# Optimization experiments

Measured on AMD Instinct MI355X. Metric: run time of the kernel, lower is better.

## Reference

```python
import jax, jax.numpy as jnp
import numpy as np

UNITS = 1024
IN_DIM = 1024
BATCH = 64
SEQ = 512


def setup_inputs() -> dict:
    key = jax.random.key(0)
    k_x, k_wf, k_wb = jax.random.split(key, 3)
    x = jax.random.normal(k_x, (BATCH, SEQ, IN_DIM), dtype=jnp.float32)
    # keras 'random_normal' initializer -> stddev 0.05
    W_fwd = jax.random.normal(k_wf, (IN_DIM + UNITS, 4 * UNITS), dtype=jnp.float32) * 0.05
    b_fwd = jnp.zeros((4 * UNITS,), dtype=jnp.float32)
    W_bwd = jax.random.normal(k_wb, (IN_DIM + UNITS, 4 * UNITS), dtype=jnp.float32) * 0.05
    b_bwd = jnp.zeros((4 * UNITS,), dtype=jnp.float32)
    return {"x": x, "W_fwd": W_fwd, "b_fwd": b_fwd, "W_bwd": W_bwd, "b_bwd": b_bwd}


def _lstm_scan(x_tbd, W, b, units, reverse):
    # x_tbd: [T, B, D] time-major
    B = x_tbd.shape[1]
    h0 = jnp.zeros((B, units), dtype=x_tbd.dtype)
    c0 = jnp.zeros((B, units), dtype=x_tbd.dtype)

    def step(carry, x_t):
        h, c = carry
        z = jnp.concatenate([x_t, h], axis=-1) @ W + b  # [B, 4U]
        zi, zf, zo, zg = jnp.split(z, 4, axis=-1)
        c_new = jax.nn.sigmoid(zf) * c + jax.nn.sigmoid(zi) * jnp.tanh(zg)
        h_new = jax.nn.sigmoid(zo) * jnp.tanh(c_new)
        return (h_new, c_new), h_new

    _, hs = jax.lax.scan(step, (h0, c0), x_tbd, reverse=reverse)
    return hs  # [T, B, U], aligned with input time order


def reference(x, W_fwd, b_fwd, W_bwd, b_bwd):
    x_tbd = jnp.transpose(x, (1, 0, 2))  # [T, B, D]
    h_fwd = _lstm_scan(x_tbd, W_fwd, b_fwd, UNITS, reverse=False)
    h_bwd = _lstm_scan(x_tbd, W_bwd, b_bwd, UNITS, reverse=True)
    h = jnp.concatenate([h_fwd, h_bwd], axis=-1)  # [T, B, 2U]
    return jnp.transpose(h, (1, 0, 2))  # [B, T, 2U]
```

## Files before the change

kernel.cpp:

```cpp
#include <hip/hip_runtime.h>
#include <stdint.h>

#define B_ 64
#define T_ 512
#define D_ 1024
#define U_ 1024
#define G4_ 4096
#define M_ (B_ * T_)

typedef unsigned short u16;
typedef float f32x4 __attribute__((ext_vector_type(4)));
typedef _Float16 f16x8 __attribute__((ext_vector_type(8)));
typedef unsigned short u16x4 __attribute__((ext_vector_type(4)));

__device__ __forceinline__ u16 f2h(float f) {
  union { _Float16 h; u16 u; } v; v.h = (_Float16)f; return v.u;
}
__device__ __forceinline__ float h2f(u16 u) {
  union { _Float16 h; u16 u; } v; v.u = u; return (float)v.h;
}
__device__ __forceinline__ float sigm(float x) { return 1.f / (1.f + __expf(-x)); }
__device__ __forceinline__ float tanhf_(float x) {
  x = fminf(12.f, fmaxf(-12.f, x));
  float e = __expf(2.f * x);
  return (e - 1.f) / (e + 1.f);
}

__device__ __forceinline__ void glds16(const void* g, void* l) {
  __builtin_amdgcn_global_load_lds(
      (const __attribute__((address_space(1))) uint32_t*)g,
      (__attribute__((address_space(3))) uint32_t*)l, 16, 0, 0);
}

template <int R>
__device__ __forceinline__ void stage_tile(const char* gbase, long gs, char* lds, int tid) {
  const int lane = tid & 63, wid = tid >> 6;
#pragma unroll
  for (int j = wid; j < R / 8; j += 4) {
    const int row = j * 8 + (lane >> 3);
    const int lg = ((lane & 7) * 16) ^ ((row & 7) << 4);
    glds16(gbase + (long)row * gs + lg, lds + j * 1024);
  }
}

__device__ __forceinline__ f16x8 read_frag(const char* lds, int row, int kbyte) {
  const int ph = row * 128 + (kbyte ^ ((row & 7) << 4));
  return *(const f16x8*)(lds + ph);
}

#define MFMA_(a, b, c) __builtin_amdgcn_mfma_f32_16x16x32_f16(a, b, c, 0, 0, 0)

#define BAR_LGKM() asm volatile("s_waitcnt lgkmcnt(0)\n\ts_barrier" ::: "memory")


__global__ __launch_bounds__(256) void cast_x_kernel(const float* __restrict__ x,
                                                     u16* __restrict__ xb) {
  const long n = (long)M_ * D_ / 4;
  for (long i = (long)blockIdx.x * blockDim.x + threadIdx.x; i < n;
       i += (long)gridDim.x * blockDim.x) {
    f32x4 v = ((const f32x4*)x)[i];
    u16x4 r;
#pragma unroll
    for (int j = 0; j < 4; ++j) r[j] = f2h(v[j]);
    ((u16x4*)xb)[i] = r;
  }
}

__global__ __launch_bounds__(256) void pack_w_kernel(const float* __restrict__ Wf,
                                                     const float* __restrict__ Wb,
                                                     u16* __restrict__ wxT,
                                                     u16* __restrict__ whT) {
  const int idx = blockIdx.x * 256 + threadIdx.x;
  const int p = idx & 4095;
  const int kc = (idx >> 12) & 63;
  const int part = (idx >> 18) & 1;
  const int d = (idx >> 19) & 1;
  const float* W = d ? Wb : Wf;
  const int orig = ((p >> 4) & 3) * 1024 + ((p >> 6) << 4) + (p & 15);
  u16* dst = (part ? whT : wxT) + ((long)d * G4_ + p) * 1024 + kc * 16;
  const float* src = W + ((long)(part * 1024 + kc * 16)) * G4_ + orig;
#pragma unroll
  for (int j = 0; j < 16; ++j) dst[j] = f2h(src[(long)j * G4_]);
}

__global__ __launch_bounds__(256) void gemm_xproj2(const u16* __restrict__ xbf,
                                                   const u16* __restrict__ wT,
                                                   const float* __restrict__ bF,
                                                   const float* __restrict__ bB,
                                                   u16* __restrict__ xp2) {
  __shared__ __align__(16) char smem[64 * 1024];
  const int tid = threadIdx.x, lane = tid & 63, wid = tid >> 6;
  const int wr = wid >> 1, wc = wid & 1;
  const int tm = blockIdx.x * 128, tn = blockIdx.y * 128, d = blockIdx.z;
  const char* Ag = (const char*)xbf + (long)tm * 2048;
  const char* Bg = (const char*)wT + ((long)d * G4_ + tn) * 2048;

  f32x4 acc[4][4];
#pragma unroll
  for (int mi = 0; mi < 4; ++mi)
#pragma unroll
    for (int ni = 0; ni < 4; ++ni)
#pragma unroll
      for (int v = 0; v < 4; ++v) acc[mi][ni][v] = 0.f;

  stage_tile<128>(Ag, 2048, smem, tid);
  stage_tile<128>(Bg, 2048, smem + 32768, tid);
  __syncthreads();
  const int rA = lane & 15, kb = (lane >> 4) * 16;

  for (int cc = 0; cc < 16; ++cc) {
    const int cur = cc & 1;
    char* Ac = smem + cur * 16384;
    char* Bc = smem + 32768 + cur * 16384;
    if (cc + 1 < 16) {
      stage_tile<128>(Ag + (cc + 1) * 128, 2048, smem + (cur ^ 1) * 16384, tid);
      stage_tile<128>(Bg + (cc + 1) * 128, 2048, smem + 32768 + (cur ^ 1) * 16384, tid);
    }
    f16x8 aF[4][2], bFr[4][2];
#pragma unroll
    for (int mi = 0; mi < 4; ++mi)
#pragma unroll
      for (int ks = 0; ks < 2; ++ks)
        aF[mi][ks] = read_frag(Ac, wr * 64 + mi * 16 + rA, kb + ks * 64);
#pragma unroll
    for (int ni = 0; ni < 4; ++ni)
#pragma unroll
      for (int ks = 0; ks < 2; ++ks)
        bFr[ni][ks] = read_frag(Bc, wc * 64 + ni * 16 + rA, kb + ks * 64);
#pragma unroll
    for (int mi = 0; mi < 4; ++mi)
#pragma unroll
      for (int ni = 0; ni < 4; ++ni)
#pragma unroll
        for (int ks = 0; ks < 2; ++ks)
          acc[mi][ni] = MFMA_(aF[mi][ks], bFr[ni][ks], acc[mi][ni]);
    __syncthreads();
  }

  const float* bias = d ? bB : bF;
#pragma unroll
  for (int ni = 0; ni < 4; ++ni) {
    const int p = tn + wc * 64 + ni * 16 + rA;
    const int orig = ((p >> 4) & 3) * 1024 + ((p >> 6) << 4) + (p & 15);
    const float bv = bias[orig];
    const int ub2 = p >> 6, pl = p & 63;
#pragma unroll
    for (int mi = 0; mi < 4; ++mi) {
      const int m0 = tm + wr * 64 + mi * 16 + (lane >> 4) * 4;
#pragma unroll
      for (int v = 0; v < 4; ++v) {
        const int m = m0 + v, b = m >> 9, t = m & 511;
        xp2[((((long)d * T_ + t) * 64 + ub2) * 64 + b) * 64 + pl] =
            f2h(acc[mi][ni][v] + bv);
      }
    }
  }
}

__global__ __launch_bounds__(512) void lstm_persist(
    const u16* __restrict__ whT, const u16* __restrict__ xp2,
    u16* __restrict__ hst, float* __restrict__ out, uint32_t* flags) {
  __shared__ __align__(16) char smem[147456];
  float* zbuf = (float*)(smem + 131072);
  const int tid = threadIdx.x, lane = tid & 63, wid = tid >> 6;
  const int bx = blockIdx.x, d = bx & 1, ub = bx >> 1;
  const int wm = wid & 3, kh = wid >> 2, rA = lane & 15, kq = lane >> 4;

  {
    const char* wbase = (const char*)(whT + ((long)d * G4_ + ub * 64) * 1024);
#pragma unroll
    for (int q = 0; q < 16; ++q) {
      const int idx = wid * 16 + q;
      const int row = idx >> 1;
      const int jl = (idx & 1) * 1024 + lane * 16;
      glds16(wbase + (long)row * 2048 + (jl ^ ((row & 7) << 4)), smem + idx * 1024);
    }
  }
  asm volatile("s_waitcnt vmcnt(0)" ::: "memory");
  __syncthreads();

  const int b_g = tid >> 3, up_g = tid & 7;
  const int u_g = ub * 16 + up_g * 2;
  float creg0 = 0.f, creg1 = 0.f;
  uint32_t* fl = flags + (long)d * 64 * 4;

  for (int s = 0; s < T_; ++s) {
    const int t = d ? (T_ - 1 - s) : s;

    if (wid == 0) {
      const uint32_t* fp = fl + lane * 4;
      int it = 0;
      while (true) {
        uint32_t v;
        asm volatile("global_load_dword %0, %1, off sc0 sc1\n\ts_waitcnt vmcnt(0)"
                     : "=v"(v) : "v"(fp) : "memory");
        if (__all(v >= (uint32_t)s)) break;
        __builtin_amdgcn_s_sleep(1);
        if (++it > (1 << 17)) break;
      }
    }
    BAR_LGKM();

    const u16* hr = hst + (long)(s & 1) * 131072 + d * 65536;
    const char* abase =
        (const char*)(hr + ((long)(wm * 16 + rA)) * 1024) + kh * 1024 + kq * 16;
    f16x8 areg[16];
#define ALOAD(i)                                                        \
  asm volatile("global_load_dwordx4 %0, %1, off offset:%2 sc0 sc1"     \
               : "=v"(areg[i]) : "v"(abase), "n"(i * 64) : "memory")
    ALOAD(0); ALOAD(1); ALOAD(2); ALOAD(3);
    ALOAD(4); ALOAD(5); ALOAD(6); ALOAD(7);
    ALOAD(8); ALOAD(9); ALOAD(10); ALOAD(11);
    ALOAD(12); ALOAD(13); ALOAD(14); ALOAD(15);
#undef ALOAD
    const u16* xb0 = xp2 + ((((long)d * T_ + t) * 64 + ub) * 64 + b_g) * 64 + up_g * 2;
    uint32_t xr[4];
#define XLOAD(g)                                                        \
  asm volatile("global_load_dword %0, %1, off offset:%2"               \
               : "=v"(xr[g]) : "v"(xb0), "n"(g * 32) : "memory")
    XLOAD(0); XLOAD(1); XLOAD(2); XLOAD(3);
#undef XLOAD
    asm volatile("s_waitcnt vmcnt(4)" ::: "memory");
    __builtin_amdgcn_sched_barrier(0);

    f32x4 acc[4];
#pragma unroll
    for (int ni = 0; ni < 4; ++ni)
#pragma unroll
      for (int v = 0; v < 4; ++v) acc[ni][v] = 0.f;
#pragma unroll
    for (int kk = 0; kk < 16; ++kk) {
      const int kbyte = kh * 1024 + kk * 64 + kq * 16;
#pragma unroll
      for (int ni = 0; ni < 4; ++ni) {
        const int pi = ni * 16 + rA;
        const f16x8 bF =
            *(const f16x8*)(smem + pi * 2048 + (kbyte ^ ((pi & 7) << 4)));
        acc[ni] = MFMA_(areg[kk], bF, acc[ni]);
      }
    }

    if (kh == 1) {
#pragma unroll
      for (int ni = 0; ni < 4; ++ni)
#pragma unroll
        for (int v = 0; v < 4; ++v)
          zbuf[(wm * 16 + kq * 4 + v) * 64 + ni * 16 + rA] = acc[ni][v];
    }
    BAR_LGKM();
    if (kh == 0) {
#pragma unroll
      for (int ni = 0; ni < 4; ++ni)
#pragma unroll
        for (int v = 0; v < 4; ++v) {
          const int ix = (wm * 16 + kq * 4 + v) * 64 + ni * 16 + rA;
          zbuf[ix] += acc[ni][v];
        }
    }
    BAR_LGKM();

    asm volatile("s_waitcnt vmcnt(0)" ::: "memory");
    __builtin_amdgcn_sched_barrier(0);

    const float* zb = zbuf + b_g * 64 + up_g * 2;
    const float zi0 = zb[0]  + h2f((u16)(xr[0] & 0xffff));
    const float zi1 = zb[1]  + h2f((u16)(xr[0] >> 16));
    const float zf0 = zb[16] + h2f((u16)(xr[1] & 0xffff));
    const float zf1 = zb[17] + h2f((u16)(xr[1] >> 16));
    const float zo0 = zb[32] + h2f((u16)(xr[2] & 0xffff));
    const float zo1 = zb[33] + h2f((u16)(xr[2] >> 16));
    const float zg0 = zb[48] + h2f((u16)(xr[3] & 0xffff));
    const float zg1 = zb[49] + h2f((u16)(xr[3] >> 16));
    const float cn0 = sigm(zf0) * creg0 + sigm(zi0) * tanhf_(zg0);
    const float cn1 = sigm(zf1) * creg1 + sigm(zi1) * tanhf_(zg1);
    const float hn0 = sigm(zo0) * tanhf_(cn0);
    const float hn1 = sigm(zo1) * tanhf_(cn1);
    creg0 = cn0; creg1 = cn1;

    u16* hw = hst + (long)((s + 1) & 1) * 131072 + d * 65536;
    const uint32_t hv = (uint32_t)f2h(hn0) | ((uint32_t)f2h(hn1) << 16);
    u16* hptr = hw + (long)b_g * 1024 + u_g;
    asm volatile("global_store_dword %0, %1, off sc0 sc1"
                 :: "v"(hptr), "v"(hv) : "memory");
    asm volatile("s_waitcnt vmcnt(0)" ::: "memory");
    BAR_LGKM();
    if (tid == 0) {
      const uint32_t fv = (uint32_t)(s + 1);
      uint32_t* fp2 = fl + ub * 4;
      asm volatile("global_store_dword %0, %1, off sc0 sc1"
                   :: "v"(fp2), "v"(fv) : "memory");
    }

    float2 o2; o2.x = hn0; o2.y = hn1;
    *(float2*)(out + ((long)b_g * T_ + t) * 2048 + d * 1024 + u_g) = o2;
  }
}

__global__ __launch_bounds__(256) void lstm_step_fused(
    const u16* __restrict__ whT, const u16* __restrict__ wxT,
    const u16* __restrict__ xbf,
    const float* __restrict__ bF, const float* __restrict__ bB,
    const u16* __restrict__ h_read, u16* __restrict__ h_write,
    float* __restrict__ c_state, float* __restrict__ out, int s) {
  __shared__ __align__(16) char smem[32 * 1024];
  float* zbuf = (float*)smem;
  const int tid = threadIdx.x, lane = tid & 63, wid = tid >> 6;
  const int wr = wid >> 1, wc = wid & 1;
  const int ub = blockIdx.x, d = blockIdx.y;
  const int t = d ? (T_ - 1 - s) : s;
  const char* hA = (const char*)(h_read + (long)d * B_ * U_);
  const char* Bh = (const char*)(whT + ((long)d * G4_ + ub * 64) * 1024);
  const char* xA = (const char*)xbf + (long)t * (D_ * 2);
  const char* Bx = (const char*)(wxT + ((long)d * G4_ + ub * 64) * 1024);

  auto stage = [&](int cc, int buf) {
    char* Ad = smem + buf * 8192;
    char* Bd = smem + 16384 + buf * 8192;
    if (cc < 16) {
      stage_tile<64>(hA + cc * 128, U_ * 2, Ad, tid);
      stage_tile<64>(Bh + cc * 128, 1024 * 2, Bd, tid);
    } else {
      const int cx = cc - 16;
      stage_tile<64>(xA + cx * 128, (long)T_ * D_ * 2, Ad, tid);
      stage_tile<64>(Bx + cx * 128, 1024 * 2, Bd, tid);
    }
  };

  f32x4 acc[2][2];
#pragma unroll
  for (int mi = 0; mi < 2; ++mi)
#pragma unroll
    for (int ni = 0; ni < 2; ++ni)
#pragma unroll
      for (int v = 0; v < 4; ++v) acc[mi][ni][v] = 0.f;

  stage(0, 0);
  __syncthreads();
  const int rA = lane & 15, kb = (lane >> 4) * 16;

  for (int cc = 0; cc < 32; ++cc) {
    const int cur = cc & 1;
    char* Ac = smem + cur * 8192;
    char* Bc = smem + 16384 + cur * 8192;
    if (cc + 1 < 32) stage(cc + 1, cur ^ 1);
    f16x8 aF[2][2], bFr[2][2];
#pragma unroll
    for (int mi = 0; mi < 2; ++mi)
#pragma unroll
      for (int ks = 0; ks < 2; ++ks)
        aF[mi][ks] = read_frag(Ac, wr * 32 + mi * 16 + rA, kb + ks * 64);
#pragma unroll
    for (int ni = 0; ni < 2; ++ni)
#pragma unroll
      for (int ks = 0; ks < 2; ++ks)
        bFr[ni][ks] = read_frag(Bc, wc * 32 + ni * 16 + rA, kb + ks * 64);
#pragma unroll
    for (int mi = 0; mi < 2; ++mi)
#pragma unroll
      for (int ni = 0; ni < 2; ++ni)
#pragma unroll
        for (int ks = 0; ks < 2; ++ks)
          acc[mi][ni] = MFMA_(aF[mi][ks], bFr[ni][ks], acc[mi][ni]);
    __syncthreads();
  }

#pragma unroll
  for (int mi = 0; mi < 2; ++mi)
#pragma unroll
    for (int ni = 0; ni < 2; ++ni)
#pragma unroll
      for (int v = 0; v < 4; ++v) {
        const int row = wr * 32 + mi * 16 + (lane >> 4) * 4 + v;
        const int col = wc * 32 + ni * 16 + rA;
        zbuf[row * 64 + col] = acc[mi][ni][v];
      }
  __syncthreads();

  const int b = tid >> 2, u0 = (tid & 3) * 4;
  const float* bias = d ? bB : bF;
#pragma unroll
  for (int j = 0; j < 4; ++j) {
    const int ui = u0 + j, u = ub * 16 + ui;
    float zi = zbuf[b * 64 + ui] + bias[u];
    float zf = zbuf[b * 64 + 16 + ui] + bias[1024 + u];
    float zo = zbuf[b * 64 + 32 + ui] + bias[2048 + u];
    float zg = zbuf[b * 64 + 48 + ui] + bias[3072 + u];
    const long ci = (((long)d * B_ + b) << 10) + u;
    const float c = c_state[ci];
    const float i_ = sigm(zi), ff = sigm(zf), o_ = sigm(zo), g_ = tanhf_(zg);
    const float cn = ff * c + i_ * g_;
    const float hn = o_ * tanhf_(cn);
    c_state[ci] = cn;
    h_write[ci] = f2h(hn);
    out[(((long)b * T_ + t) << 11) + ((long)d << 10) + u] = hn;
  }
}


extern "C" void kernel_launch(void* const* d_in, const int* in_sizes, int n_in,
                              void* d_out, int out_size, void* d_ws, size_t ws_size,
                              hipStream_t stream) {
  const float* x = (const float*)d_in[0];
  const float* Wf = (const float*)d_in[1];
  const float* bfp = (const float*)d_in[2];
  const float* Wb = (const float*)d_in[3];
  const float* bbp = (const float*)d_in[4];
  float* out = (float*)d_out;
  char* ws = (char*)d_ws;

  size_t off = 0;
  auto alloc = [&](size_t bytes) {
    char* p = ws + off;
    off = (off + bytes + 255) & ~(size_t)255;
    return p;
  };
  u16* xbf = (u16*)alloc((size_t)M_ * D_ * 2);
  u16* wxT = (u16*)alloc((size_t)2 * G4_ * 1024 * 2);
  u16* whT = (u16*)alloc((size_t)2 * G4_ * 1024 * 2);
  u16* hst = (u16*)alloc((size_t)2 * 2 * B_ * U_ * 2);
  float* cst = (float*)alloc((size_t)2 * B_ * U_ * 4);
  uint32_t* flags = (uint32_t*)alloc((size_t)2 * 64 * 16 * 4);
  const size_t base_need = off;
  const size_t xproj_bytes = (size_t)2 * B_ * T_ * G4_ * 2;
  const bool fused = (ws_size < base_need + xproj_bytes + 256);
  u16* xproj = fused ? nullptr : (u16*)alloc(xproj_bytes);

  hipMemsetAsync(hst, 0, (size_t)2 * 2 * B_ * U_ * 2, stream);
  hipMemsetAsync(flags, 0, (size_t)2 * 64 * 16 * 4, stream);

  cast_x_kernel<<<2048, 256, 0, stream>>>(x, xbf);
  pack_w_kernel<<<4096, 256, 0, stream>>>(Wf, Wb, wxT, whT);

  if (!fused) {
    dim3 gg(M_ / 128, G4_ / 128, 2);
    gemm_xproj2<<<gg, 256, 0, stream>>>(xbf, wxT, bfp, bbp, xproj);
    lstm_persist<<<128, 512, 0, stream>>>(whT, xproj, hst, out, flags);
  } else {
    hipMemsetAsync(cst, 0, (size_t)2 * B_ * U_ * 4, stream);
    for (int s = 0; s < T_; ++s) {
      const u16* hr = hst + (size_t)(s & 1) * 2 * B_ * U_;
      u16* hw = hst + (size_t)((s + 1) & 1) * 2 * B_ * U_;
      lstm_step_fused<<<dim3(64, 2), 256, 0, stream>>>(whT, wxT, xbf, bfp, bbp,
                                                       hr, hw, cst, out, s);
    }
  }
}
```

Baseline: 4.451 ms.

## Version hidden-state buffers per step and relayout recurrent weights in LDS

```diff
diff --git a/kernel.cpp b/kernel.cpp
--- a/kernel.cpp
+++ b/kernel.cpp
@@ -157,10 +157,12 @@
   }
 }
 
+#define ZLD 65
+template <int VER>
 __global__ __launch_bounds__(512) void lstm_persist(
     const u16* __restrict__ whT, const u16* __restrict__ xp2,
     u16* __restrict__ hst, float* __restrict__ out, uint32_t* flags) {
-  __shared__ __align__(16) char smem[147456];
+  __shared__ __align__(16) char smem[131072 + ZLD * 64 * 4];
   float* zbuf = (float*)(smem + 131072);
   const int tid = threadIdx.x, lane = tid & 63, wid = tid >> 6;
   const int bx = blockIdx.x, d = bx & 1, ub = bx >> 1;
@@ -170,10 +172,11 @@
     const char* wbase = (const char*)(whT + ((long)d * G4_ + ub * 64) * 1024);
 #pragma unroll
     for (int q = 0; q < 16; ++q) {
-      const int idx = wid * 16 + q;
-      const int row = idx >> 1;
-      const int jl = (idx & 1) * 1024 + lane * 16;
-      glds16(wbase + (long)row * 2048 + (jl ^ ((row & 7) << 4)), smem + idx * 1024);
+      const int f = wid * 16 + q;
+      const int ni = f >> 5, kkg = f & 31;
+      const int row = ni * 16 + (lane & 15);
+      glds16(wbase + (long)row * 2048 + kkg * 64 + (lane >> 4) * 16,
+             smem + f * 1024);
     }
   }
   asm volatile("s_waitcnt vmcnt(0)" ::: "memory");
@@ -186,6 +189,14 @@
 
   for (int s = 0; s < T_; ++s) {
     const int t = d ? (T_ - 1 - s) : s;
+
+    const u16* xb0 = xp2 + ((((long)d * T_ + t) * 64 + ub) * 64 + b_g) * 64 + up_g * 2;
+    uint32_t xr[4];
+#define XLOAD(g)                                                        \
+  asm volatile("global_load_dword %0, %1, off offset:%2"               \
+               : "=v"(xr[g]) : "v"(xb0), "n"(g * 32) : "memory")
+    XLOAD(0); XLOAD(1); XLOAD(2); XLOAD(3);
+#undef XLOAD
 
     if (wid == 0) {
       const uint32_t* fp = fl + lane * 4;
@@ -201,26 +212,31 @@
     }
     BAR_LGKM();
 
-    const u16* hr = hst + (long)(s & 1) * 131072 + d * 65536;
+    const u16* hr = hst + (VER ? (long)s * 131072 : (long)(s & 1) * 131072)
+                    + (long)d * 65536;
     const char* abase =
         (const char*)(hr + ((long)(wm * 16 + rA)) * 1024) + kh * 1024 + kq * 16;
     f16x8 areg[16];
-#define ALOAD(i)                                                        \
+#define ALOADC(i)                                                       \
+  asm volatile("global_load_dwordx4 %0, %1, off offset:%2"             \
+               : "=v"(areg[i]) : "v"(abase), "n"(i * 64) : "memory")
+#define ALOADU(i)                                                       \
   asm volatile("global_load_dwordx4 %0, %1, off offset:%2 sc0 sc1"     \
                : "=v"(areg[i]) : "v"(abase), "n"(i * 64) : "memory")
-    ALOAD(0); ALOAD(1); ALOAD(2); ALOAD(3);
-    ALOAD(4); ALOAD(5); ALOAD(6); ALOAD(7);
-    ALOAD(8); ALOAD(9); ALOAD(10); ALOAD(11);
-    ALOAD(12); ALOAD(13); ALOAD(14); ALOAD(15);
-#undef ALOAD
-    const u16* xb0 = xp2 + ((((long)d * T_ + t) * 64 + ub) * 64 + b_g) * 64 + up_g * 2;
-    uint32_t xr[4];
-#define XLOAD(g)                                                        \
-  asm volatile("global_load_dword %0, %1, off offset:%2"               \
-               : "=v"(xr[g]) : "v"(xb0), "n"(g * 32) : "memory")
-    XLOAD(0); XLOAD(1); XLOAD(2); XLOAD(3);
-#undef XLOAD
-    asm volatile("s_waitcnt vmcnt(4)" ::: "memory");
+    if (VER) {
+      ALOADC(0); ALOADC(1); ALOADC(2); ALOADC(3);
+      ALOADC(4); ALOADC(5); ALOADC(6); ALOADC(7);
+      ALOADC(8); ALOADC(9); ALOADC(10); ALOADC(11);
+      ALOADC(12); ALOADC(13); ALOADC(14); ALOADC(15);
+    } else {
+      ALOADU(0); ALOADU(1); ALOADU(2); ALOADU(3);
+      ALOADU(4); ALOADU(5); ALOADU(6); ALOADU(7);
+      ALOADU(8); ALOADU(9); ALOADU(10); ALOADU(11);
+      ALOADU(12); ALOADU(13); ALOADU(14); ALOADU(15);
+    }
+#undef ALOADC
+#undef ALOADU
+    asm volatile("s_waitcnt vmcnt(0)" ::: "memory");
     __builtin_amdgcn_sched_barrier(0);
 
     f32x4 acc[4];
@@ -228,14 +244,12 @@
     for (int ni = 0; ni < 4; ++ni)
 #pragma unroll
       for (int v = 0; v < 4; ++v) acc[ni][v] = 0.f;
+    const char* bbase = smem + (kh << 14) + (lane << 4);
 #pragma unroll
     for (int kk = 0; kk < 16; ++kk) {
-      const int kbyte = kh * 1024 + kk * 64 + kq * 16;
 #pragma unroll
       for (int ni = 0; ni < 4; ++ni) {
-        const int pi = ni * 16 + rA;
-        const f16x8 bF =
-            *(const f16x8*)(smem + pi * 2048 + (kbyte ^ ((pi & 7) << 4)));
+        const f16x8 bF = *(const f16x8*)(bbase + (ni << 15) + (kk << 10));
         acc[ni] = MFMA_(areg[kk], bF, acc[ni]);
       }
     }
@@ -245,7 +259,7 @@
       for (int ni = 0; ni < 4; ++ni)
 #pragma unroll
         for (int v = 0; v < 4; ++v)
-          zbuf[(wm * 16 + kq * 4 + v) * 64 + ni * 16 + rA] = acc[ni][v];
+          zbuf[(wm * 16 + kq * 4 + v) * ZLD + ni * 16 + rA] = acc[ni][v];
     }
     BAR_LGKM();
     if (kh == 0) {
@@ -253,16 +267,13 @@
       for (int ni = 0; ni < 4; ++ni)
 #pragma unroll
         for (int v = 0; v < 4; ++v) {
-          const int ix = (wm * 16 + kq * 4 + v) * 64 + ni * 16 + rA;
+          const int ix = (wm * 16 + kq * 4 + v) * ZLD + ni * 16 + rA;
           zbuf[ix] += acc[ni][v];
         }
     }
     BAR_LGKM();
 
-    asm volatile("s_waitcnt vmcnt(0)" ::: "memory");
-    __builtin_amdgcn_sched_barrier(0);
-
-    const float* zb = zbuf + b_g * 64 + up_g * 2;
+    const float* zb = zbuf + b_g * ZLD + up_g * 2;
     const float zi0 = zb[0]  + h2f((u16)(xr[0] & 0xffff));
     const float zi1 = zb[1]  + h2f((u16)(xr[0] >> 16));
     const float zf0 = zb[16] + h2f((u16)(xr[1] & 0xffff));
@@ -277,7 +288,8 @@
     const float hn1 = sigm(zo1) * tanhf_(cn1);
     creg0 = cn0; creg1 = cn1;
 
-    u16* hw = hst + (long)((s + 1) & 1) * 131072 + d * 65536;
+    u16* hw = hst + (VER ? (long)(s + 1) * 131072 : (long)((s + 1) & 1) * 131072)
+              + (long)d * 65536;
     const uint32_t hv = (uint32_t)f2h(hn0) | ((uint32_t)f2h(hn1) << 16);
     u16* hptr = hw + (long)b_g * 1024 + u_g;
     asm volatile("global_store_dword %0, %1, off sc0 sc1"
@@ -414,27 +426,35 @@
     off = (off + bytes + 255) & ~(size_t)255;
     return p;
   };
+  const size_t hst_ver_bytes = (size_t)(T_ + 1) * 2 * B_ * U_ * 2;
+  const size_t hst_pp_bytes = (size_t)2 * 2 * B_ * U_ * 2;
+  const size_t xproj_bytes = (size_t)2 * B_ * T_ * G4_ * 2;
+  const size_t fixed = (size_t)M_ * D_ * 2 + 2 * ((size_t)2 * G4_ * 1024 * 2) +
+                       (size_t)2 * B_ * U_ * 4 + (size_t)2 * 64 * 16 * 4 + 4096;
+  const bool versioned = ws_size >= fixed + hst_ver_bytes + xproj_bytes + 4096;
+  const bool fusedp = ws_size < fixed + hst_pp_bytes + xproj_bytes + 4096;
+
   u16* xbf = (u16*)alloc((size_t)M_ * D_ * 2);
   u16* wxT = (u16*)alloc((size_t)2 * G4_ * 1024 * 2);
   u16* whT = (u16*)alloc((size_t)2 * G4_ * 1024 * 2);
-  u16* hst = (u16*)alloc((size_t)2 * 2 * B_ * U_ * 2);
+  u16* hst = (u16*)alloc(versioned ? hst_ver_bytes : hst_pp_bytes);
   float* cst = (float*)alloc((size_t)2 * B_ * U_ * 4);
   uint32_t* flags = (uint32_t*)alloc((size_t)2 * 64 * 16 * 4);
-  const size_t base_need = off;
-  const size_t xproj_bytes = (size_t)2 * B_ * T_ * G4_ * 2;
-  const bool fused = (ws_size < base_need + xproj_bytes + 256);
-  u16* xproj = fused ? nullptr : (u16*)alloc(xproj_bytes);
-
-  hipMemsetAsync(hst, 0, (size_t)2 * 2 * B_ * U_ * 2, stream);
+  u16* xproj = fusedp ? nullptr : (u16*)alloc(xproj_bytes);
+
+  hipMemsetAsync(hst, 0, versioned ? (size_t)2 * B_ * U_ * 2 : hst_pp_bytes, stream);
   hipMemsetAsync(flags, 0, (size_t)2 * 64 * 16 * 4, stream);
 
   cast_x_kernel<<<2048, 256, 0, stream>>>(x, xbf);
   pack_w_kernel<<<4096, 256, 0, stream>>>(Wf, Wb, wxT, whT);
 
-  if (!fused) {
+  if (!fusedp) {
     dim3 gg(M_ / 128, G4_ / 128, 2);
     gemm_xproj2<<<gg, 256, 0, stream>>>(xbf, wxT, bfp, bbp, xproj);
-    lstm_persist<<<128, 512, 0, stream>>>(whT, xproj, hst, out, flags);
+    if (versioned)
+      lstm_persist<1><<<128, 512, 0, stream>>>(whT, xproj, hst, out, flags);
+    else
+      lstm_persist<0><<<128, 512, 0, stream>>>(whT, xproj, hst, out, flags);
   } else {
     hipMemsetAsync(cst, 0, (size_t)2 * B_ * U_ * 4, stream);
     for (int s = 0; s < T_; ++s) {
```

Measured after the change: 4.580 ms. +2.9%, slower.

## Replace per-step barriers with LDS token spin-waits and fuse gate math into MFMA waves

Applied to the files above, without the earlier changes.

```diff
diff --git a/kernel.cpp b/kernel.cpp
--- a/kernel.cpp
+++ b/kernel.cpp
@@ -16,8 +16,8 @@
 __device__ __forceinline__ u16 f2h(float f) {
   union { _Float16 h; u16 u; } v; v.h = (_Float16)f; return v.u;
 }
-__device__ __forceinline__ float h2f(u16 u) {
-  union { _Float16 h; u16 u; } v; v.u = u; return (float)v.h;
+__device__ __forceinline__ float h2f(uint32_t u) {
+  union { _Float16 h; u16 u; } v; v.u = (u16)u; return (float)v.h;
 }
 __device__ __forceinline__ float sigm(float x) { return 1.f / (1.f + __expf(-x)); }
 __device__ __forceinline__ float tanhf_(float x) {
@@ -49,7 +49,6 @@
 }
 
 #define MFMA_(a, b, c) __builtin_amdgcn_mfma_f32_16x16x32_f16(a, b, c, 0, 0, 0)
-
 #define BAR_LGKM() asm volatile("s_waitcnt lgkmcnt(0)\n\ts_barrier" ::: "memory")
 
 
@@ -61,7 +60,7 @@
     f32x4 v = ((const f32x4*)x)[i];
     u16x4 r;
 #pragma unroll
-    for (int j = 0; j < 4; ++j) r[j] = f2h(v[j]);
+    for (int j = 0; j < 4; ++j) { union { _Float16 h; u16 u; } c; c.h = (_Float16)v[j]; r[j] = c.u; }
     ((u16x4*)xb)[i] = r;
   }
 }
@@ -157,49 +156,76 @@
   }
 }
 
+#define ZLD 65
 __global__ __launch_bounds__(512) void lstm_persist(
     const u16* __restrict__ whT, const u16* __restrict__ xp2,
     u16* __restrict__ hst, float* __restrict__ out, uint32_t* flags) {
-  __shared__ __align__(16) char smem[147456];
+  __shared__ __align__(16) char smem[131072 + ZLD * 64 * 4 + 16];
   float* zbuf = (float*)(smem + 131072);
+  int* tok = (int*)(smem + 131072 + ZLD * 64 * 4);
   const int tid = threadIdx.x, lane = tid & 63, wid = tid >> 6;
   const int bx = blockIdx.x, d = bx & 1, ub = bx >> 1;
   const int wm = wid & 3, kh = wid >> 2, rA = lane & 15, kq = lane >> 4;
 
+  if (tid == 0) { tok[0] = -1; tok[1] = -1; tok[2] = 0; }
+
   {
     const char* wbase = (const char*)(whT + ((long)d * G4_ + ub * 64) * 1024);
 #pragma unroll
     for (int q = 0; q < 16; ++q) {
-      const int idx = wid * 16 + q;
-      const int row = idx >> 1;
-      const int jl = (idx & 1) * 1024 + lane * 16;
-      glds16(wbase + (long)row * 2048 + (jl ^ ((row & 7) << 4)), smem + idx * 1024);
+      const int f = wid * 16 + q;
+      const int ni = f >> 5, kkg = f & 31;
+      const int row = ni * 16 + (lane & 15);
+      glds16(wbase + (long)row * 2048 + kkg * 64 + (lane >> 4) * 16,
+             smem + f * 1024);
     }
   }
   asm volatile("s_waitcnt vmcnt(0)" ::: "memory");
   __syncthreads();
 
-  const int b_g = tid >> 3, up_g = tid & 7;
-  const int u_g = ub * 16 + up_g * 2;
-  float creg0 = 0.f, creg1 = 0.f;
+  const int u_g = ub * 16 + rA;
+  const int row0 = wm * 16 + kq * 4;
+  f32x4 creg;
+#pragma unroll
+  for (int v = 0; v < 4; ++v) creg[v] = 0.f;
   uint32_t* fl = flags + (long)d * 64 * 4;
 
   for (int s = 0; s < T_; ++s) {
     const int t = d ? (T_ - 1 - s) : s;
 
-    if (wid == 0) {
-      const uint32_t* fp = fl + lane * 4;
+    uint32_t xr[4][4];
+    if (kh == 0) {
+      const char* xpb = (const char*)(xp2 + (((long)d * T_ + t) * 64 + ub) * 4096);
+#pragma unroll
+      for (int v = 0; v < 4; ++v) {
+        const char* bp = xpb + ((row0 + v) * 64 + rA) * 2;
+#define XL(g)                                                            \
+  asm volatile("global_load_ushort %0, %1, off offset:%2"                \
+               : "=v"(xr[v][g]) : "v"(bp), "n"(g * 32) : "memory")
+        XL(0); XL(1); XL(2); XL(3);
+#undef XL
+      }
+    }
+
+    if (wid == 0 || wid == 4) {
+      const uint32_t* fp = fl + ((lane & 31) + kh * 32) * 4;
       int it = 0;
       while (true) {
         uint32_t v;
         asm volatile("global_load_dword %0, %1, off sc0 sc1\n\ts_waitcnt vmcnt(0)"
                      : "=v"(v) : "v"(fp) : "memory");
         if (__all(v >= (uint32_t)s)) break;
-        __builtin_amdgcn_s_sleep(1);
         if (++it > (1 << 17)) break;
       }
-    }
-    BAR_LGKM();
+      __hip_atomic_store(tok + kh, s, __ATOMIC_RELAXED, __HIP_MEMORY_SCOPE_WORKGROUP);
+    }
+    {
+      int it = 0;
+      while (__hip_atomic_load(tok + kh, __ATOMIC_RELAXED,
+                               __HIP_MEMORY_SCOPE_WORKGROUP) < s) {
+        if (++it > (1 << 20)) break;
+      }
+    }
 
     const u16* hr = hst + (long)(s & 1) * 131072 + d * 65536;
     const char* abase =
@@ -213,14 +239,7 @@
     ALOAD(8); ALOAD(9); ALOAD(10); ALOAD(11);
     ALOAD(12); ALOAD(13); ALOAD(14); ALOAD(15);
 #undef ALOAD
-    const u16* xb0 = xp2 + ((((long)d * T_ + t) * 64 + ub) * 64 + b_g) * 64 + up_g * 2;
-    uint32_t xr[4];
-#define XLOAD(g)                                                        \
-  asm volatile("global_load_dword %0, %1, off offset:%2"               \
-               : "=v"(xr[g]) : "v"(xb0), "n"(g * 32) : "memory")
-    XLOAD(0); XLOAD(1); XLOAD(2); XLOAD(3);
-#undef XLOAD
-    asm volatile("s_waitcnt vmcnt(4)" ::: "memory");
+    asm volatile("s_waitcnt vmcnt(0)" ::: "memory");
     __builtin_amdgcn_sched_barrier(0);
 
     f32x4 acc[4];
@@ -228,14 +247,12 @@
     for (int ni = 0; ni < 4; ++ni)
 #pragma unroll
       for (int v = 0; v < 4; ++v) acc[ni][v] = 0.f;
+    const char* bbase = smem + (kh << 14) + (lane << 4);
 #pragma unroll
     for (int kk = 0; kk < 16; ++kk) {
-      const int kbyte = kh * 1024 + kk * 64 + kq * 16;
 #pragma unroll
       for (int ni = 0; ni < 4; ++ni) {
-        const int pi = ni * 16 + rA;
-        const f16x8 bF =
-            *(const f16x8*)(smem + pi * 2048 + (kbyte ^ ((pi & 7) << 4)));
+        const f16x8 bF = *(const f16x8*)(bbase + (ni << 15) + (kk << 10));
         acc[ni] = MFMA_(areg[kk], bF, acc[ni]);
       }
     }
@@ -245,54 +262,58 @@
       for (int ni = 0; ni < 4; ++ni)
 #pragma unroll
         for (int v = 0; v < 4; ++v)
-          zbuf[(wm * 16 + kq * 4 + v) * 64 + ni * 16 + rA] = acc[ni][v];
+          zbuf[(row0 + v) * ZLD + ni * 16 + rA] = acc[ni][v];
     }
     BAR_LGKM();
     if (kh == 0) {
 #pragma unroll
       for (int ni = 0; ni < 4; ++ni)
 #pragma unroll
-        for (int v = 0; v < 4; ++v) {
-          const int ix = (wm * 16 + kq * 4 + v) * 64 + ni * 16 + rA;
-          zbuf[ix] += acc[ni][v];
+        for (int v = 0; v < 4; ++v)
+          acc[ni][v] += zbuf[(row0 + v) * ZLD + ni * 16 + rA];
+    }
+    BAR_LGKM();
+
+    if (kh == 0) {
+      float hn[4];
+#pragma unroll
+      for (int v = 0; v < 4; ++v) {
+        const float zi = acc[0][v] + h2f(xr[v][0]);
+        const float zf = acc[1][v] + h2f(xr[v][1]);
+        const float zo = acc[2][v] + h2f(xr[v][2]);
+        const float zg = acc[3][v] + h2f(xr[v][3]);
+        const float cn = sigm(zf) * creg[v] + sigm(zi) * tanhf_(zg);
+        hn[v] = sigm(zo) * tanhf_(cn);
+        creg[v] = cn;
+      }
+      u16* hw = hst + (long)((s + 1) & 1) * 131072 + d * 65536;
+#pragma unroll
+      for (int v = 0; v < 4; ++v) {
+        union { _Float16 h; u16 u; } cv; cv.h = (_Float16)hn[v];
+        const uint32_t hv = cv.u;
+        u16* hp = hw + (long)(row0 + v) * 1024 + u_g;
+        asm volatile("global_store_short %0, %1, off sc0 sc1"
+                     :: "v"(hp), "v"(hv) : "memory");
+      }
+      asm volatile("s_waitcnt vmcnt(0)" ::: "memory");
+      if (lane == 0)
+        __hip_atomic_fetch_add(tok + 2, 1, __ATOMIC_RELAXED,
+                               __HIP_MEMORY_SCOPE_WORKGROUP);
+      if (tid == 0) {
+        int it = 0;
+        while (__hip_atomic_load(tok + 2, __ATOMIC_RELAXED,
+                                 __HIP_MEMORY_SCOPE_WORKGROUP) < 4 * (s + 1)) {
+          if (++it > (1 << 20)) break;
         }
-    }
-    BAR_LGKM();
-
-    asm volatile("s_waitcnt vmcnt(0)" ::: "memory");
-    __builtin_amdgcn_sched_barrier(0);
-
-    const float* zb = zbuf + b_g * 64 + up_g * 2;
-    const float zi0 = zb[0]  + h2f((u16)(xr[0] & 0xffff));
-    const float zi1 = zb[1]  + h2f((u16)(xr[0] >> 16));
-    const float zf0 = zb[16] + h2f((u16)(xr[1] & 0xffff));
-    const float zf1 = zb[17] + h2f((u16)(xr[1] >> 16));
-    const float zo0 = zb[32] + h2f((u16)(xr[2] & 0xffff));
-    const float zo1 = zb[33] + h2f((u16)(xr[2] >> 16));
-    const float zg0 = zb[48] + h2f((u16)(xr[3] & 0xffff));
-    const float zg1 = zb[49] + h2f((u16)(xr[3] >> 16));
-    const float cn0 = sigm(zf0) * creg0 + sigm(zi0) * tanhf_(zg0);
-    const float cn1 = sigm(zf1) * creg1 + sigm(zi1) * tanhf_(zg1);
-    const float hn0 = sigm(zo0) * tanhf_(cn0);
-    const float hn1 = sigm(zo1) * tanhf_(cn1);
-    creg0 = cn0; creg1 = cn1;
-
-    u16* hw = hst + (long)((s + 1) & 1) * 131072 + d * 65536;
-    const uint32_t hv = (uint32_t)f2h(hn0) | ((uint32_t)f2h(hn1) << 16);
-    u16* hptr = hw + (long)b_g * 1024 + u_g;
-    asm volatile("global_store_dword %0, %1, off sc0 sc1"
-                 :: "v"(hptr), "v"(hv) : "memory");
-    asm volatile("s_waitcnt vmcnt(0)" ::: "memory");
-    BAR_LGKM();
-    if (tid == 0) {
-      const uint32_t fv = (uint32_t)(s + 1);
-      uint32_t* fp2 = fl + ub * 4;
-      asm volatile("global_store_dword %0, %1, off sc0 sc1"
-                   :: "v"(fp2), "v"(fv) : "memory");
-    }
-
-    float2 o2; o2.x = hn0; o2.y = hn1;
-    *(float2*)(out + ((long)b_g * T_ + t) * 2048 + d * 1024 + u_g) = o2;
+        const uint32_t fv = (uint32_t)(s + 1);
+        uint32_t* fp2 = fl + ub * 4;
+        asm volatile("global_store_dword %0, %1, off sc0 sc1"
+                     :: "v"(fp2), "v"(fv) : "memory");
+      }
+#pragma unroll
+      for (int v = 0; v < 4; ++v)
+        out[((long)(row0 + v) * T_ + t) * 2048 + d * 1024 + u_g] = hn[v];
+    }
   }
 }
 
```

Measured after the change: 4.797 ms. +7.8%, slower.
